# Kernel optimization log

Hardware: AMD Instinct MI355X
Metric: run time of the kernel (lower is better)

Reference implementation:

```python
import jax, jax.numpy as jnp
import numpy as np
from jax import lax

B, S, HDIM = 4, 2048, 1024
H, D, L = 16, 64, 128
NB = S // L
EPS = 1e-8


def setup_inputs() -> dict:
    key = jax.random.key(0)
    ks = jax.random.split(key, 16)
    std = 0.02
    inp = {
        'f_in': jax.random.normal(ks[0], (B, S, HDIM), jnp.float32),
        'i_in': jax.random.normal(ks[1], (B, S, HDIM), jnp.float32),
        'z_in': jax.random.normal(ks[2], (B, S, HDIM), jnp.float32),
        'o_in': jax.random.normal(ks[3], (B, S, HDIM), jnp.float32),
        'c0': jax.random.normal(ks[4], (B, H, D), jnp.float32),
        'h0': jax.random.normal(ks[5], (B, H, D), jnp.float32),
        # weights stored (in, out) so forward is x @ W + b
        'Wf': std * jax.random.normal(ks[6], (HDIM, H * D), jnp.float32),
        'bf': jnp.zeros((H * D,), jnp.float32),
        'Wi': std * jax.random.normal(ks[7], (HDIM, H * D), jnp.float32),
        'bi': jnp.zeros((H * D,), jnp.float32),
        'Wz': std * jax.random.normal(ks[8], (HDIM, H * D), jnp.float32),
        'bz': jnp.zeros((H * D,), jnp.float32),
        'Wo': std * jax.random.normal(ks[9], (HDIM, H * D), jnp.float32),
        'bo': jnp.zeros((H * D,), jnp.float32),
        'Wp': std * jax.random.normal(ks[10], (H * D, HDIM), jnp.float32),
        'bp': jnp.zeros((HDIM,), jnp.float32),
    }
    return inp


def _to_blocks(x):
    # (B,S,H*D) -> (NB, B, H, D, L), matching torch view+permute(1,0,3,4,2)
    return jnp.transpose(x.reshape(B, NB, L, H, D), (1, 0, 3, 4, 2))


def _qlstm(f_in, i_in, z_in, o_in, c0, Wf, bf, Wi, bi, Wz, bz, Wo, bo, Wp, bp):
    fx = _to_blocks(f_in @ Wf + bf)
    ix = _to_blocks(i_in @ Wi + bi)
    zx = _to_blocks(z_in @ Wz + bz)
    ox = _to_blocks(o_in @ Wo + bo)

    f = jax.nn.sigmoid(fx + 1.0)              # (NB,B,H,D,L)
    o = jax.nn.sigmoid(ox)
    update = jax.nn.sigmoid(ix) * jnp.tanh(zx)

    kk = jnp.arange(L)[:, None]
    ll = jnp.arange(L + 1)[None, :]
    ones_mask = ll >= kk + 1                   # (L, L+1): filled with 1.0
    zeros_mask = ll >= kk + 2                  # (L, L+1): zeroed out

    def block_step(c, blk):
        fb, ob, ub = blk                       # each (B,H,D,L)
        cf = jnp.concatenate([fb, jnp.ones(fb.shape[:-1] + (1,), fb.dtype)], axis=-1)  # (B,H,D,L+1)
        Fm = jnp.broadcast_to(cf[..., None, :], fb.shape[:-1] + (L, L + 1))
        Fm = jnp.where(ones_mask, 1.0, Fm)
        # reversed log-cumsum-exp along last axis (decay products)
        Fm = jnp.exp(jnp.flip(jnp.cumsum(jnp.flip(jnp.log(Fm + EPS), -1), -1), -1)) - EPS
        Fm = jnp.where(zeros_mask, 0.0, Fm)    # (B,H,D,L,L+1)
        u = jnp.concatenate([c[..., None], ub], axis=-1)   # (B,H,D,L+1)
        cs = jnp.einsum('bhdkl,bhdl->bhdk', Fm, u)          # (B,H,D,L)
        hs = ob * jnp.tanh(cs)
        return cs[..., -1], hs

    last_c, hs = lax.scan(block_step, c0, (f, o, update))   # hs: (NB,B,H,D,L)
    last_h = hs[-1, ..., -1]
    y = jnp.transpose(hs, (1, 0, 4, 2, 3)).reshape(B, S, H * D)
    y = y @ Wp + bp                            # (B,S,HDIM)
    return y, last_c, last_h


def reference(f_in, i_in, z_in, o_in, c0, h0, Wf, bf, Wi, bi, Wz, bz, Wo, bo, Wp, bp):
    y, last_c, last_h = _qlstm(f_in, i_in, z_in, o_in, c0,
                               Wf, bf, Wi, bi, Wz, bz, Wo, bo, Wp, bp)
    return y, last_c, last_h
```

## Files before the change

### kernel.cpp

```cpp
#include <hip/hip_runtime.h>
#include <hip/hip_bf16.h>
#include <stdint.h>

constexpr int GM = 8192;
constexpr int GK = 1024;
constexpr int GN = 1024;
constexpr size_t NACT = (size_t)GM * GN;
constexpr int CHUNK = 32;
constexpr int NCHUNK = 64;
constexpr int NCH = 4096;
constexpr int NT = GK / 64;

#define DEVINL __device__ __forceinline__

typedef __attribute__((ext_vector_type(8))) short bf16x8;
typedef __attribute__((ext_vector_type(4))) float f32x4;

DEVINL float sigmoidf_(float x) { return 1.0f / (1.0f + __expf(-x)); }

DEVINL unsigned short f2bf(float x) {
  unsigned int u = __builtin_bit_cast(unsigned int, x);
  unsigned int rnd = 0x7fffu + ((u >> 16) & 1u);
  return (unsigned short)((u + rnd) >> 16);
}
DEVINL float bf2f(unsigned short u) {
  unsigned int x = ((unsigned int)u) << 16;
  return __builtin_bit_cast(float, x);
}

DEVINL void gload16(const void* g, void* l) {
  __builtin_amdgcn_global_load_lds(
      (const __attribute__((address_space(1))) unsigned int*)g,
      (__attribute__((address_space(3))) unsigned int*)l, 16, 0, 0);
}

__global__ void cvt4_kernel(const float* __restrict__ s0, const float* __restrict__ s1,
                            const float* __restrict__ s2, const float* __restrict__ s3,
                            unsigned short* __restrict__ d0, unsigned short* __restrict__ d1,
                            unsigned short* __restrict__ d2, unsigned short* __restrict__ d3,
                            int n4) {
  const float* s;
  unsigned short* d;
  switch (blockIdx.y) {
    case 0: s = s0; d = d0; break;
    case 1: s = s1; d = d1; break;
    case 2: s = s2; d = d2; break;
    default: s = s3; d = d3; break;
  }
  int stride = gridDim.x * blockDim.x;
  for (int i = blockIdx.x * blockDim.x + threadIdx.x; i < n4; i += stride) {
    float4 v = ((const float4*)s)[i];
    ushort4 o;
    o.x = f2bf(v.x); o.y = f2bf(v.y); o.z = f2bf(v.z); o.w = f2bf(v.w);
    ((ushort4*)d)[i] = o;
  }
}

struct TPtrs {
  const float* src[5];
  unsigned short* dst[5];
};

__global__ void transpose_cvt_all(TPtrs p) {
  const float* __restrict__ W = p.src[blockIdx.z];
  unsigned short* __restrict__ Wt = p.dst[blockIdx.z];
  __shared__ float tile[32][33];
  int n0 = blockIdx.x * 32, k0 = blockIdx.y * 32;
  int tx = threadIdx.x & 31, ty = threadIdx.x >> 5;
#pragma unroll
  for (int i = 0; i < 32; i += 8)
    tile[ty + i][tx] = W[(size_t)(k0 + ty + i) * GN + n0 + tx];
  __syncthreads();
#pragma unroll
  for (int i = 0; i < 32; i += 8)
    Wt[(size_t)(n0 + ty + i) * GK + k0 + tx] = f2bf(tile[tx][ty + i]);
}

DEVINL void gemm256_core(const unsigned short* __restrict__ A,
                         const unsigned short* __restrict__ W,
                         char* lds, int tid, int wave, int lane,
                         int bm, int bn, f32x4 (&acc)[8][4]) {
  const char* Ag = (const char*)A;
  const char* Wg = (const char*)W;
  const int Ah = wave >> 2;
  const int wn = (wave & 3) * 64;
  const int lrow = lane & 15;
  const int lgrp = lane >> 4;

  auto stage = [&](int buf, int tk) {
#pragma unroll
    for (int hh = 0; hh < 4; ++hh) {
#pragma unroll
      for (int j = 0; j < 2; ++j) {
        const int lbyte = j * 8192 + tid * 16;
        const int row = lbyte >> 7;
        const int gcb = (lbyte & 127) ^ ((row & 7) << 4);
        const char* src = (hh < 2)
            ? Ag + (size_t)(bm * 256 + hh * 128 + row) * 2048 + tk * 128 + gcb
            : Wg + (size_t)(bn * 256 + (hh - 2) * 128 + row) * 2048 + tk * 128 + gcb;
        char* dst = lds + buf * 65536 + (hh >= 2 ? 32768 : 0) + (hh & 1) * 16384 +
                    j * 8192 + wave * 1024;
        gload16(src, dst);
      }
    }
  };

  stage(0, 0);

  for (int t = 0; t < NT; ++t) {
    const int cur = t & 1;
    const char* Abase = lds + cur * 65536 + Ah * 16384;
    const char* Bbase = lds + cur * 65536 + 32768;

    stage(cur ^ 1, t + 1);
    asm volatile("s_waitcnt vmcnt(8)" ::: "memory");
    __builtin_amdgcn_sched_barrier(0);
    __builtin_amdgcn_s_barrier();
    __builtin_amdgcn_sched_barrier(0);

    bf16x8 aF[4][2], bF[4][2];
#pragma unroll
    for (int m = 0; m < 4; ++m)
#pragma unroll
      for (int ks = 0; ks < 2; ++ks) {
        const int r = m * 16 + lrow;
        const int cb = ks * 64 + lgrp * 16;
        aF[m][ks] = *(const bf16x8*)(Abase + r * 128 + (cb ^ ((r & 7) << 4)));
      }
#pragma unroll
    for (int n = 0; n < 2; ++n)
#pragma unroll
      for (int ks = 0; ks < 2; ++ks) {
        const int nr = wn + n * 16 + lrow;
        const int cb = ks * 64 + lgrp * 16;
        bF[n][ks] = *(const bf16x8*)(Bbase + nr * 128 + (cb ^ ((nr & 7) << 4)));
      }
    __builtin_amdgcn_s_setprio(1);
#pragma unroll
    for (int m = 0; m < 4; ++m)
#pragma unroll
      for (int n = 0; n < 2; ++n)
#pragma unroll
        for (int ks = 0; ks < 2; ++ks)
          acc[m][n] = __builtin_amdgcn_mfma_f32_16x16x32_bf16(aF[m][ks], bF[n][ks],
                                                              acc[m][n], 0, 0, 0);
    __builtin_amdgcn_s_setprio(0);
    __builtin_amdgcn_sched_barrier(0);
    __builtin_amdgcn_s_barrier();
    __builtin_amdgcn_sched_barrier(0);

#pragma unroll
    for (int n = 2; n < 4; ++n)
#pragma unroll
      for (int ks = 0; ks < 2; ++ks) {
        const int nr = wn + n * 16 + lrow;
        const int cb = ks * 64 + lgrp * 16;
        bF[n][ks] = *(const bf16x8*)(Bbase + nr * 128 + (cb ^ ((nr & 7) << 4)));
      }
    __builtin_amdgcn_s_setprio(1);
#pragma unroll
    for (int m = 0; m < 4; ++m)
#pragma unroll
      for (int n = 2; n < 4; ++n)
#pragma unroll
        for (int ks = 0; ks < 2; ++ks)
          acc[m][n] = __builtin_amdgcn_mfma_f32_16x16x32_bf16(aF[m][ks], bF[n][ks],
                                                              acc[m][n], 0, 0, 0);
    __builtin_amdgcn_s_setprio(0);
    __builtin_amdgcn_sched_barrier(0);
    __builtin_amdgcn_s_barrier();
    __builtin_amdgcn_sched_barrier(0);

#pragma unroll
    for (int m = 0; m < 4; ++m)
#pragma unroll
      for (int ks = 0; ks < 2; ++ks) {
        const int r = (m + 4) * 16 + lrow;
        const int cb = ks * 64 + lgrp * 16;
        aF[m][ks] = *(const bf16x8*)(Abase + r * 128 + (cb ^ ((r & 7) << 4)));
      }
    __builtin_amdgcn_s_setprio(1);
#pragma unroll
    for (int m = 0; m < 4; ++m)
#pragma unroll
      for (int n = 2; n < 4; ++n)
#pragma unroll
        for (int ks = 0; ks < 2; ++ks)
          acc[m + 4][n] = __builtin_amdgcn_mfma_f32_16x16x32_bf16(aF[m][ks], bF[n][ks],
                                                                  acc[m + 4][n], 0, 0, 0);
    __builtin_amdgcn_s_setprio(0);
    __builtin_amdgcn_sched_barrier(0);
    __builtin_amdgcn_s_barrier();
    __builtin_amdgcn_sched_barrier(0);

    __builtin_amdgcn_s_setprio(1);
#pragma unroll
    for (int m = 0; m < 4; ++m)
#pragma unroll
      for (int n = 0; n < 2; ++n)
#pragma unroll
        for (int ks = 0; ks < 2; ++ks)
          acc[m + 4][n] = __builtin_amdgcn_mfma_f32_16x16x32_bf16(aF[m][ks], bF[n][ks],
                                                                  acc[m + 4][n], 0, 0, 0);
    __builtin_amdgcn_s_setprio(0);
  }
}

struct GateArgs {
  const unsigned short* A[4];
  const unsigned short* W[4];
  const float* bias[4];
  unsigned short* out[4];
};

__global__ __launch_bounds__(512, 2) void gemm_gates8(GateArgs ga) {
  extern __shared__ char lds[];
  const int tid = threadIdx.x;
  const int wave = tid >> 6, lane = tid & 63;
  const int bm = blockIdx.x, bn = blockIdx.y, gz = blockIdx.z;
  const int wm = (wave >> 2) * 128, wn = (wave & 3) * 64;
  const int lrow = lane & 15, lgrp = lane >> 4;

  f32x4 acc[8][4];
#pragma unroll
  for (int m = 0; m < 8; ++m)
#pragma unroll
    for (int n = 0; n < 4; ++n) acc[m][n] = (f32x4){0.f, 0.f, 0.f, 0.f};

  gemm256_core(ga.A[gz], ga.W[gz], lds, tid, wave, lane, bm, bn, acc);

  const float* bias = ga.bias[gz];
  unsigned short* out = ga.out[gz];
  float bv[4];
#pragma unroll
  for (int n = 0; n < 4; ++n) bv[n] = bias[bn * 256 + wn + n * 16 + lrow];

#pragma unroll
  for (int m = 0; m < 8; ++m)
#pragma unroll
    for (int n = 0; n < 4; ++n) {
      const int gc = bn * 256 + wn + n * 16 + lrow;
#pragma unroll
      for (int j = 0; j < 4; ++j) {
        const int gr = bm * 256 + wm + m * 16 + lgrp * 4 + j;
        float v = acc[m][n][j] + bv[n];
        if (gz == 0) v = sigmoidf_(v + 1.0f);
        else if (gz == 1) v = sigmoidf_(v);
        out[(size_t)gr * GN + gc] = f2bf(v);
      }
    }
}

__global__ __launch_bounds__(512, 2) void gemm_proj8(
    const unsigned short* __restrict__ A, const unsigned short* __restrict__ W,
    const float* __restrict__ bias, float* __restrict__ out) {
  extern __shared__ char lds[];
  const int tid = threadIdx.x;
  const int wave = tid >> 6, lane = tid & 63;
  const int bm = blockIdx.x, bn = blockIdx.y;
  const int wm = (wave >> 2) * 128, wn = (wave & 3) * 64;
  const int lrow = lane & 15, lgrp = lane >> 4;

  f32x4 acc[8][4];
#pragma unroll
  for (int m = 0; m < 8; ++m)
#pragma unroll
    for (int n = 0; n < 4; ++n) acc[m][n] = (f32x4){0.f, 0.f, 0.f, 0.f};

  gemm256_core(A, W, lds, tid, wave, lane, bm, bn, acc);

  float bv[4];
#pragma unroll
  for (int n = 0; n < 4; ++n) bv[n] = bias[bn * 256 + wn + n * 16 + lrow];

#pragma unroll
  for (int m = 0; m < 8; ++m)
#pragma unroll
    for (int n = 0; n < 4; ++n) {
      const int gc = bn * 256 + wn + n * 16 + lrow;
#pragma unroll
      for (int j = 0; j < 4; ++j) {
        const int gr = bm * 256 + wm + m * 16 + lgrp * 4 + j;
        out[(size_t)gr * GN + gc] = acc[m][n][j] + bv[n];
      }
    }
}

__global__ void scan_phaseA_kernel(const unsigned short* __restrict__ F,
                                   const unsigned short* __restrict__ Ip,
                                   const unsigned short* __restrict__ Zp,
                                   float* __restrict__ Pt, float* __restrict__ Ct) {
  int tid = blockIdx.x * blockDim.x + threadIdx.x;
  int ch = tid & (NCH - 1), chunk = tid >> 12;
  int b = ch >> 10, n = ch & 1023;
  size_t base = ((size_t)(b * 2048 + chunk * CHUNK)) * 1024 + n;
  float c = 0.f, P = 1.f;
#pragma unroll 8
  for (int t = 0; t < CHUNK; ++t) {
    size_t idx = base + (size_t)t * 1024;
    float f = bf2f(F[idx]);
    float u = sigmoidf_(bf2f(Ip[idx])) * tanhf(bf2f(Zp[idx]));
    c = __builtin_fmaf(f, c, u);
    P *= f;
  }
  Pt[tid] = P;
  Ct[tid] = c;
}

__global__ void scan_combine_kernel(const float* __restrict__ Pt,
                                    const float* __restrict__ Ct,
                                    const float* __restrict__ c0,
                                    float* __restrict__ Cin,
                                    float* __restrict__ last_c) {
  int ch = blockIdx.x * blockDim.x + threadIdx.x;
  float c = c0[ch];
#pragma unroll
  for (int j = 0; j < NCHUNK; ++j) {
    Cin[j * NCH + ch] = c;
    c = __builtin_fmaf(Pt[j * NCH + ch], c, Ct[j * NCH + ch]);
  }
  last_c[ch] = c;
}

__global__ void scan_phaseC_kernel(const unsigned short* __restrict__ F,
                                   const unsigned short* __restrict__ Ip,
                                   const unsigned short* __restrict__ Zp,
                                   const unsigned short* __restrict__ O,
                                   const float* __restrict__ Cin,
                                   unsigned short* __restrict__ Hb,
                                   float* __restrict__ last_h) {
  int tid = blockIdx.x * blockDim.x + threadIdx.x;
  int ch = tid & (NCH - 1), chunk = tid >> 12;
  int b = ch >> 10, n = ch & 1023;
  size_t base = ((size_t)(b * 2048 + chunk * CHUNK)) * 1024 + n;
  float c = Cin[tid];
  float h = 0.f;
#pragma unroll 8
  for (int t = 0; t < CHUNK; ++t) {
    size_t idx = base + (size_t)t * 1024;
    float f = bf2f(F[idx]);
    float u = sigmoidf_(bf2f(Ip[idx])) * tanhf(bf2f(Zp[idx]));
    float o = bf2f(O[idx]);
    c = __builtin_fmaf(f, c, u);
    h = o * tanhf(c);
    Hb[idx] = f2bf(h);
  }
  if (chunk == NCHUNK - 1) last_h[ch] = h;
}

extern "C" void kernel_launch(void* const* d_in, const int* in_sizes, int n_in,
                              void* d_out, int out_size, void* d_ws, size_t ws_size,
                              hipStream_t stream) {
  const float* f_in = (const float*)d_in[0];
  const float* i_in = (const float*)d_in[1];
  const float* z_in = (const float*)d_in[2];
  const float* o_in = (const float*)d_in[3];
  const float* c0 = (const float*)d_in[4];
  const float* Wf = (const float*)d_in[6];
  const float* bf_ = (const float*)d_in[7];
  const float* Wi = (const float*)d_in[8];
  const float* bi = (const float*)d_in[9];
  const float* Wz = (const float*)d_in[10];
  const float* bz = (const float*)d_in[11];
  const float* Wo = (const float*)d_in[12];
  const float* bo = (const float*)d_in[13];
  const float* Wp = (const float*)d_in[14];
  const float* bp = (const float*)d_in[15];

  float* y = (float*)d_out;
  float* last_c = y + NACT;
  float* last_h = last_c + NCH;

  char* w = (char*)d_ws;
  const size_t ABYTES = NACT * 2;
  const size_t WBYTES = (size_t)GK * GN * 2;
  unsigned short* Af = (unsigned short*)(w + 0 * ABYTES);
  unsigned short* Ai = (unsigned short*)(w + 1 * ABYTES);
  unsigned short* Az = (unsigned short*)(w + 2 * ABYTES);
  unsigned short* Ao = (unsigned short*)(w + 3 * ABYTES);
  char* wt = w + 4 * ABYTES;
  unsigned short* Wtf = (unsigned short*)(wt + 0 * WBYTES);
  unsigned short* Wti = (unsigned short*)(wt + 1 * WBYTES);
  unsigned short* Wtz = (unsigned short*)(wt + 2 * WBYTES);
  unsigned short* Wto = (unsigned short*)(wt + 3 * WBYTES);
  unsigned short* Wtp = (unsigned short*)(wt + 4 * WBYTES);
  char* gp = wt + 5 * WBYTES;
  unsigned short* F = (unsigned short*)(gp + 0 * ABYTES);
  unsigned short* O = (unsigned short*)(gp + 1 * ABYTES);
  unsigned short* Ip = (unsigned short*)(gp + 2 * ABYTES);
  unsigned short* Zp = (unsigned short*)(gp + 3 * ABYTES);
  unsigned short* Hb = Af;
  char* sp = gp + 4 * ABYTES;
  const size_t SBYTES = (size_t)NCH * NCHUNK * 4;
  float* Pt = (float*)(sp + 0 * SBYTES);
  float* Ct = (float*)(sp + 1 * SBYTES);
  float* Cin = (float*)(sp + 2 * SBYTES);

  (void)hipFuncSetAttribute((const void*)gemm_gates8,
                            hipFuncAttributeMaxDynamicSharedMemorySize, 131072);
  (void)hipFuncSetAttribute((const void*)gemm_proj8,
                            hipFuncAttributeMaxDynamicSharedMemorySize, 131072);

  cvt4_kernel<<<dim3(1024, 4), 256, 0, stream>>>(
      f_in, o_in, i_in, z_in, Af, Ao, Ai, Az, (int)(NACT / 4));

  TPtrs tp;
  tp.src[0] = Wf; tp.src[1] = Wi; tp.src[2] = Wz; tp.src[3] = Wo; tp.src[4] = Wp;
  tp.dst[0] = Wtf; tp.dst[1] = Wti; tp.dst[2] = Wtz; tp.dst[3] = Wto; tp.dst[4] = Wtp;
  transpose_cvt_all<<<dim3(32, 32, 5), 256, 0, stream>>>(tp);

  GateArgs ga;
  ga.A[0] = Af;  ga.A[1] = Ao;  ga.A[2] = Ai;  ga.A[3] = Az;
  ga.W[0] = Wtf; ga.W[1] = Wto; ga.W[2] = Wti; ga.W[3] = Wtz;
  ga.bias[0] = bf_; ga.bias[1] = bo; ga.bias[2] = bi; ga.bias[3] = bz;
  ga.out[0] = F; ga.out[1] = O; ga.out[2] = Ip; ga.out[3] = Zp;
  gemm_gates8<<<dim3(GM / 256, GN / 256, 4), 512, 131072, stream>>>(ga);

  scan_phaseA_kernel<<<(NCH * NCHUNK) / 256, 256, 0, stream>>>(F, Ip, Zp, Pt, Ct);
  scan_combine_kernel<<<NCH / 256, 256, 0, stream>>>(Pt, Ct, c0, Cin, last_c);
  scan_phaseC_kernel<<<(NCH * NCHUNK) / 256, 256, 0, stream>>>(F, Ip, Zp, O, Cin, Hb,
                                                               last_h);

  gemm_proj8<<<dim3(GM / 256, GN / 256), 512, 131072, stream>>>(Hb, Wtp, bp, y);
}
```

Before: 217.2 us.

## Split GEMM prefetch into two halves interleaved with MFMA phases

Global-to-LDS source and destination addresses are now computed once before the loop instead of every tile. The next tile's prefetch is split into two groups of four loads, issued at different MFMA phases, with the vmcnt wait relaxed and barrier placement reorganised. The aim is to spread memory issue across the compute phases and cut address arithmetic and some scheduling barriers. This risks LDS read/write races if the barrier placement is wrong, and the last iteration redundantly reloads the final tile.

```diff
diff --git a/kernel.cpp b/kernel.cpp
--- a/kernel.cpp
+++ b/kernel.cpp
@@ -80,45 +80,50 @@
                          const unsigned short* __restrict__ W,
                          char* lds, int tid, int wave, int lane,
                          int bm, int bn, f32x4 (&acc)[8][4]) {
-  const char* Ag = (const char*)A;
-  const char* Wg = (const char*)W;
   const int Ah = wave >> 2;
   const int wn = (wave & 3) * 64;
   const int lrow = lane & 15;
   const int lgrp = lane >> 4;
 
-  auto stage = [&](int buf, int tk) {
-#pragma unroll
-    for (int hh = 0; hh < 4; ++hh) {
+  const char* gsrc[8];
+  char* ldst[8];
+  {
+    const char* Ag = (const char*)A;
+    const char* Wg = (const char*)W;
+#pragma unroll
+    for (int hh = 0; hh < 4; ++hh)
 #pragma unroll
       for (int j = 0; j < 2; ++j) {
         const int lbyte = j * 8192 + tid * 16;
         const int row = lbyte >> 7;
         const int gcb = (lbyte & 127) ^ ((row & 7) << 4);
-        const char* src = (hh < 2)
-            ? Ag + (size_t)(bm * 256 + hh * 128 + row) * 2048 + tk * 128 + gcb
-            : Wg + (size_t)(bn * 256 + (hh - 2) * 128 + row) * 2048 + tk * 128 + gcb;
-        char* dst = lds + buf * 65536 + (hh >= 2 ? 32768 : 0) + (hh & 1) * 16384 +
-                    j * 8192 + wave * 1024;
-        gload16(src, dst);
-      }
-    }
-  };
-
-  stage(0, 0);
+        const int i = hh * 2 + j;
+        gsrc[i] = (hh < 2)
+            ? Ag + (size_t)(bm * 256 + hh * 128 + row) * 2048 + gcb
+            : Wg + (size_t)(bn * 256 + (hh - 2) * 128 + row) * 2048 + gcb;
+        ldst[i] = lds + (hh >= 2 ? 32768 : 0) + (hh & 1) * 16384 + j * 8192 +
+                  wave * 1024;
+      }
+  }
+
+#pragma unroll
+  for (int i = 0; i < 8; ++i) gload16(gsrc[i], ldst[i]);
+
+  bf16x8 aF[4][2], bF[4][2];
 
   for (int t = 0; t < NT; ++t) {
     const int cur = t & 1;
+    const int obuf = (cur ^ 1) * 65536;
     const char* Abase = lds + cur * 65536 + Ah * 16384;
     const char* Bbase = lds + cur * 65536 + 32768;
-
-    stage(cur ^ 1, t + 1);
-    asm volatile("s_waitcnt vmcnt(8)" ::: "memory");
-    __builtin_amdgcn_sched_barrier(0);
+    const int nk = (t + 1 < NT) ? (t + 1) : (NT - 1);
+    const size_t koff = (size_t)nk * 128;
+
+#pragma unroll
+    for (int i = 0; i < 4; ++i) gload16(gsrc[i] + koff, ldst[i] + obuf);
+    asm volatile("s_waitcnt vmcnt(4)" ::: "memory");
     __builtin_amdgcn_s_barrier();
     __builtin_amdgcn_sched_barrier(0);
-
-    bf16x8 aF[4][2], bF[4][2];
 #pragma unroll
     for (int m = 0; m < 4; ++m)
 #pragma unroll
@@ -145,9 +150,6 @@
           acc[m][n] = __builtin_amdgcn_mfma_f32_16x16x32_bf16(aF[m][ks], bF[n][ks],
                                                               acc[m][n], 0, 0, 0);
     __builtin_amdgcn_s_setprio(0);
-    __builtin_amdgcn_sched_barrier(0);
-    __builtin_amdgcn_s_barrier();
-    __builtin_amdgcn_sched_barrier(0);
 
 #pragma unroll
     for (int n = 2; n < 4; ++n)
@@ -157,6 +159,11 @@
         const int cb = ks * 64 + lgrp * 16;
         bF[n][ks] = *(const bf16x8*)(Bbase + nr * 128 + (cb ^ ((nr & 7) << 4)));
       }
+#pragma unroll
+    for (int i = 4; i < 8; ++i) gload16(gsrc[i] + koff, ldst[i] + obuf);
+    __builtin_amdgcn_s_barrier();
+    asm volatile("s_waitcnt lgkmcnt(0)" ::: "memory");
+    __builtin_amdgcn_sched_barrier(0);
     __builtin_amdgcn_s_setprio(1);
 #pragma unroll
     for (int m = 0; m < 4; ++m)
@@ -167,9 +174,6 @@
           acc[m][n] = __builtin_amdgcn_mfma_f32_16x16x32_bf16(aF[m][ks], bF[n][ks],
                                                               acc[m][n], 0, 0, 0);
     __builtin_amdgcn_s_setprio(0);
-    __builtin_amdgcn_sched_barrier(0);
-    __builtin_amdgcn_s_barrier();
-    __builtin_amdgcn_sched_barrier(0);
 
 #pragma unroll
     for (int m = 0; m < 4; ++m)
@@ -179,6 +183,9 @@
         const int cb = ks * 64 + lgrp * 16;
         aF[m][ks] = *(const bf16x8*)(Abase + r * 128 + (cb ^ ((r & 7) << 4)));
       }
+    __builtin_amdgcn_s_barrier();
+    asm volatile("s_waitcnt lgkmcnt(0)" ::: "memory");
+    __builtin_amdgcn_sched_barrier(0);
     __builtin_amdgcn_s_setprio(1);
 #pragma unroll
     for (int m = 0; m < 4; ++m)
@@ -189,10 +196,8 @@
           acc[m + 4][n] = __builtin_amdgcn_mfma_f32_16x16x32_bf16(aF[m][ks], bF[n][ks],
                                                                   acc[m + 4][n], 0, 0, 0);
     __builtin_amdgcn_s_setprio(0);
-    __builtin_amdgcn_sched_barrier(0);
+
     __builtin_amdgcn_s_barrier();
-    __builtin_amdgcn_sched_barrier(0);
-
     __builtin_amdgcn_s_setprio(1);
 #pragma unroll
     for (int m = 0; m < 4; ++m)
```

Result: faster. 206.1 us (-5.1%).
